# Optimization experiments

Measured on AMD Instinct MI355X. Metric: run time of the kernel, lower is better.

The kernel has to match this reference:

```python
import jax, jax.numpy as jnp
import numpy as np

B, L, HIDDEN = 64, 200, 256
HEADS = 8
MAX_WIDTH = 5
EPS = 1e-5  # F.layer_norm default eps


def _ln(x):
    # F.layer_norm with no learned affine
    m = jnp.mean(x, axis=-1, keepdims=True)
    v = jnp.mean((x - m) ** 2, axis=-1, keepdims=True)
    return (x - m) * jax.lax.rsqrt(v + EPS)


def _area_pool(x, max_width, mode):
    # x: [B, H, L, D] -> pooled spans of widths 1..max_width (valid windows),
    # concatenated along the memory axis: M = sum_w (L - w + 1)
    Lx = x.shape[2]
    outs = []
    for w in range(1, max_width + 1):
        # [w, B, H, L-w+1, D] stack of shifted slices (w <= 5, tiny loop)
        win = jnp.stack([x[:, :, i:Lx - w + 1 + i, :] for i in range(w)], axis=0)
        if mode == 'max':
            outs.append(win.max(axis=0))
        elif mode == 'mean':
            outs.append(win.mean(axis=0))
        else:  # 'sum'
            outs.append(win.sum(axis=0))
    return jnp.concatenate(outs, axis=2)


def _mha_area(q_in, k_in, v_in, Wq, bq, Wk, bk, Wv, bv, Wo, bo):
    # per-head size equals hidden_size (key_query_size_hidden = hidden_size)
    Bq, Lq, _ = q_in.shape
    Dh = Wq.shape[1] // HEADS

    def split(x):
        return x.reshape(x.shape[0], x.shape[1], HEADS, Dh).transpose(0, 2, 1, 3)

    q = split(q_in @ Wq + bq)  # [B, H, Lq, Dh]
    k = split(k_in @ Wk + bk)
    v = split(v_in @ Wv + bv)
    k_area = _area_pool(k, MAX_WIDTH, 'max')   # aggr='max' key pooling
    v_area = _area_pool(v, MAX_WIDTH, 'sum')   # values pooled by sum (t2t default)
    scale = jnp.asarray(1.0 / np.sqrt(Dh), q.dtype)
    logits = jnp.einsum('bhqd,bhmd->bhqm', q, k_area) * scale
    attn = jax.nn.softmax(logits, axis=-1)  # dropout inactive at eval
    out = jnp.einsum('bhqm,bhmd->bhqd', attn, v_area)
    out = out.transpose(0, 2, 1, 3).reshape(Bq, Lq, HEADS * Dh)
    return out @ Wo + bo


def setup_inputs() -> dict:
    key = jax.random.key(0)
    ks = jax.random.split(key, 16)
    stdv = 1.0 / np.sqrt(HIDDEN)
    u = lambda k, shp: jax.random.uniform(k, shp, jnp.float32, -stdv, stdv)
    HD = HEADS * HIDDEN  # 2048
    return {
        'A': jax.random.normal(ks[0], (B, L, L), jnp.float32),
        'hidden': jax.random.normal(ks[1], (B, L, HIDDEN), jnp.float32),
        'Wq': u(ks[2], (HIDDEN, HD)), 'bq': u(ks[3], (HD,)),
        'Wk': u(ks[4], (HIDDEN, HD)), 'bk': u(ks[5], (HD,)),
        'Wv': u(ks[6], (HIDDEN, HD)), 'bv': u(ks[7], (HD,)),
        'Wo': u(ks[8], (HD, HIDDEN)), 'bo': u(ks[9], (HIDDEN,)),
        'W1': u(ks[10], (HIDDEN, 4 * HIDDEN)), 'b1': u(ks[11], (4 * HIDDEN,)),
        'W2': u(ks[12], (4 * HIDDEN, HIDDEN)), 'b2': u(ks[13], (HIDDEN,)),
    }


def reference(A, hidden, Wq, bq, Wk, bk, Wv, bv, Wo, bo, W1, b1, W2, b2):
    # step = 1 -> single ATTNCell; A is unused by ATTNCell (matches source)
    attn1 = _mha_area(hidden, hidden, hidden, Wq, bq, Wk, bk, Wv, bv, Wo, bo)
    attn1 = _ln(attn1 + hidden)
    attn2 = _mha_area(attn1, hidden, hidden, Wq, bq, Wk, bk, Wv, bv, Wo, bo)
    attn2 = _ln(attn1 + attn2)  # F.dropout inactive (eval)
    x = jax.nn.relu(attn2 @ W1 + b1) @ W2 + b2
    return _ln(attn2 + x)
```

## Files before the change

kernel.cpp:

```cpp
#include <hip/hip_runtime.h>
#include <hip/hip_bf16.h>
#include <cstdint>
#include <cstddef>

#define BATCH 64
#define LSEQ 200
#define HID 256
#define NH 8
#define DH 256
#define HD (NH*DH)
#define MROWS (BATCH*LSEQ)
#define EPS 1e-5f
#define CSCALE 0.09014195f

typedef unsigned short ushort_t;
typedef __attribute__((ext_vector_type(8))) short bf16x8;
typedef __attribute__((ext_vector_type(8))) unsigned short u16x8;
typedef __attribute__((ext_vector_type(4))) float f32x4;

__device__ __forceinline__ float b2f(ushort_t u) {
    union { unsigned int i; float f; } c; c.i = ((unsigned int)u) << 16; return c.f;
}
__device__ __forceinline__ ushort_t f2b(float f) {
    __hip_bfloat16 h = __float2bfloat16(f);
    union { __hip_bfloat16 h; ushort_t u; } c; c.h = h; return c.u;
}
__device__ __forceinline__ ushort_t f2b_trunc(float f) {
    return (ushort_t)(__float_as_uint(f) >> 16);
}
__device__ __forceinline__ float to_f32(float x) { return x; }
__device__ __forceinline__ float to_f32(ushort_t x) { return b2f(x); }
__device__ __forceinline__ void store_val(float* p, float v) { *p = v; }
__device__ __forceinline__ void store_val(ushort_t* p, float v) { *p = f2b(v); }

__device__ __forceinline__ u16x8 bmax8(u16x8 a, u16x8 b) {
    union U { u16x8 v; __hip_bfloat162 h[4]; };
    U ua, ub, r; ua.v = a; ub.v = b;
    #pragma unroll
    for (int i = 0; i < 4; ++i) r.h[i] = __hmax2(ua.h[i], ub.h[i]);
    return r.v;
}
__device__ __forceinline__ u16x8 badd8(u16x8 a, u16x8 b) {
    union U { u16x8 v; __hip_bfloat162 h[4]; };
    U ua, ub, r; ua.v = a; ub.v = b;
    #pragma unroll
    for (int i = 0; i < 4; ++i) r.h[i] = __hadd2(ua.h[i], ub.h[i]);
    return r.v;
}

__device__ __forceinline__ void gll16(const void* g, void* l) {
    __builtin_amdgcn_global_load_lds(
        (const __attribute__((address_space(1))) unsigned int*)g,
        (__attribute__((address_space(3))) unsigned int*)l, 16, 0, 0);
}

template<bool RELU, int OMODE, bool SCALEC>
__global__ __launch_bounds__(256) void gemm_bt(
    const ushort_t* __restrict__ A, const ushort_t* __restrict__ Bt,
    const float* __restrict__ bias, ushort_t* __restrict__ C,
    int M, int N, int K)
{
    __shared__ ushort_t As[128 * 32];
    __shared__ ushort_t Bs[128 * 32];
    const int t = threadIdx.x;
    const int m0 = blockIdx.y * 128, n0 = blockIdx.x * 128;
    const int wave = t >> 6, lane = t & 63;
    const int l15 = lane & 15, lq = lane >> 4;
    const int wr = wave >> 1, wc = wave & 1;

    f32x4 acc[4][4];
    #pragma unroll
    for (int i = 0; i < 4; ++i)
        #pragma unroll
        for (int j = 0; j < 4; ++j) acc[i][j] = (f32x4){0.f, 0.f, 0.f, 0.f};

    for (int k0 = 0; k0 < K; k0 += 32) {
        __syncthreads();
        #pragma unroll
        for (int i = 0; i < 2; ++i) {
            int li = i * 256 + t;
            int ml = li >> 2, cp = li & 3;
            int cg = cp ^ ((ml ^ (ml >> 2)) & 3);
            gll16(A + (size_t)(m0 + ml) * K + k0 + cg * 8, &As[li * 8]);
        }
        #pragma unroll
        for (int i = 0; i < 2; ++i) {
            int li = i * 256 + t;
            int nl = li >> 2, cp = li & 3;
            int cg = cp ^ ((nl ^ (nl >> 2)) & 3);
            gll16(Bt + (size_t)(n0 + nl) * K + k0 + cg * 8, &Bs[li * 8]);
        }
        __syncthreads();
        bf16x8 af[4], bfr[4];
        #pragma unroll
        for (int i = 0; i < 4; ++i) {
            int r = wr * 64 + i * 16 + l15;
            int pc = lq ^ ((r ^ (r >> 2)) & 3);
            af[i] = *(const bf16x8*)&As[r * 32 + pc * 8];
        }
        #pragma unroll
        for (int j = 0; j < 4; ++j) {
            int r = wc * 64 + j * 16 + l15;
            int pc = lq ^ ((r ^ (r >> 2)) & 3);
            bfr[j] = *(const bf16x8*)&Bs[r * 32 + pc * 8];
        }
        #pragma unroll
        for (int i = 0; i < 4; ++i)
            #pragma unroll
            for (int j = 0; j < 4; ++j)
                acc[i][j] = __builtin_amdgcn_mfma_f32_16x16x32_bf16(af[i], bfr[j], acc[i][j], 0, 0, 0);
    }
    if (OMODE == 2) {
        #pragma unroll
        for (int i = 0; i < 4; ++i) {
            int mbase = m0 + wr * 64 + i * 16 + 4 * lq;
            int bb = (int)(((unsigned)mbase * 5243u) >> 20);
            int ll = mbase - bb * 200;
            #pragma unroll
            for (int j = 0; j < 4; ++j) {
                int n = n0 + wc * 64 + j * 16 + l15;
                float bsv = bias[n];
                ushort4 o4;
                o4.x = f2b(acc[i][j][0] + bsv); o4.y = f2b(acc[i][j][1] + bsv);
                o4.z = f2b(acc[i][j][2] + bsv); o4.w = f2b(acc[i][j][3] + bsv);
                size_t addr = ((size_t)(bb * NH + (n >> 8)) * 256 + (n & 255)) * LSEQ + ll;
                *(ushort4*)&C[addr] = o4;
            }
        }
    } else {
        #pragma unroll
        for (int i = 0; i < 4; ++i) {
            #pragma unroll
            for (int e = 0; e < 4; ++e) {
                int m = m0 + wr * 64 + i * 16 + 4 * lq + e;
                #pragma unroll
                for (int j = 0; j < 4; ++j) {
                    int n = n0 + wc * 64 + j * 16 + l15;
                    float v = acc[i][j][e] + bias[n];
                    if (RELU) v = fmaxf(v, 0.f);
                    if (SCALEC) v *= CSCALE;
                    if (OMODE == 1) {
                        int bb = (int)(((unsigned)m * 5243u) >> 20);
                        int ll = m - bb * 200;
                        size_t addr = ((((size_t)(bb * NH + (n >> 8))) * LSEQ + ll) << 8) + (n & 255);
                        C[addr] = f2b(v);
                    } else {
                        C[(size_t)m * N + n] = f2b(v);
                    }
                }
            }
        }
    }
}

__global__ __launch_bounds__(512, 2) void attn_mfma11(
    const ushort_t* __restrict__ Q, const ushort_t* __restrict__ Khm,
    const ushort_t* __restrict__ Vt, ushort_t* __restrict__ O)
{
    const int id = blockIdx.x;
    const int xcd = id & 7, slot_ = id >> 3;
    const int qt = slot_ & 1;
    const int bh = ((slot_ >> 1) << 3) + xcd;
    const int b = bh >> 3, h = bh & 7;
    const int q0 = qt * 128;
    const int t = threadIdx.x;
    const int wave = t >> 6, lane = t & 63;
    const int l15 = lane & 15, lq = lane >> 4;

    __shared__ ushort_t Ks[64 * 256];
    __shared__ ushort_t Vs[256 * 64];
    __shared__ ushort_t Ps[8][16][72];

    const ushort_t* kbh = Khm + (size_t)bh * LSEQ * DH;
    const ushort_t* vtb = Vt + (size_t)bh * DH * LSEQ;
    const ushort_t* qbh = Q + ((size_t)b * LSEQ) * HD + h * DH;
    const int qrow = q0 + wave * 16 + l15;

    bf16x8 qf[8];
    if (qrow < LSEQ) {
        const ushort_t* qp = qbh + (size_t)qrow * HD + 8 * lq;
        #pragma unroll
        for (int g = 0; g < 8; ++g) qf[g] = *(const bf16x8*)(qp + 32 * g);
    } else {
        bf16x8 zf = {0,0,0,0,0,0,0,0};
        #pragma unroll
        for (int g = 0; g < 8; ++g) qf[g] = zf;
    }

    f32x4 oacc[16];
    #pragma unroll
    for (int i = 0; i < 16; ++i) oacc[i] = (f32x4){0.f, 0.f, 0.f, 0.f};
    float l_st[4];
    #pragma unroll
    for (int e = 0; e < 4; ++e) l_st[e] = 0.f;

    const int dc = t & 31, mb = t >> 5;
    const int vd = t >> 1, vh = t & 1;

    auto step = [&](bool tail) {
        f32x4 sacc[4];
        #pragma unroll
        for (int ms = 0; ms < 4; ++ms) {
            f32x4 s = (f32x4){0.f, 0.f, 0.f, 0.f};
            const int row = ms * 16 + l15;
            #pragma unroll
            for (int g = 0; g < 8; ++g) {
                const int phys = (lq + 4 * g) ^ l15;
                s = __builtin_amdgcn_mfma_f32_16x16x32_bf16(
                        qf[g], *(const bf16x8*)&Ks[row * 256 + phys * 8], s, 0, 0, 0);
            }
            sacc[ms] = s;
        }
        if (tail) {
            #pragma unroll
            for (int ms = 0; ms < 4; ++ms) {
                const int slot = ms * 16 + l15;
                const bool inval = ((slot & 7) > 7 - (slot >> 3)) || ((slot >> 3) > 4);
                #pragma unroll
                for (int e = 0; e < 4; ++e)
                    if (inval) sacc[ms][e] = -1e30f;
            }
        }
        #pragma unroll
        for (int ms = 0; ms < 4; ++ms)
            #pragma unroll
            for (int e = 0; e < 4; ++e) {
                float pj = __builtin_exp2f(sacc[ms][e]);
                l_st[e] += pj;
                Ps[wave][4 * lq + e][ms * 16 + l15] = f2b_trunc(pj);
            }

        bf16x8 pf0 = *(const bf16x8*)&Ps[wave][l15][8 * lq];
        bf16x8 pf1 = *(const bf16x8*)&Ps[wave][l15][32 + 8 * lq];
        #pragma unroll
        for (int dt = 0; dt < 16; ++dt) {
            const int d = dt * 16 + l15;
            const int p0 = lq ^ (d & 7);
            const int p1 = (lq + 4) ^ (d & 7);
            oacc[dt] = __builtin_amdgcn_mfma_f32_16x16x32_bf16(
                           pf0, *(const bf16x8*)&Vs[d * 64 + p0 * 8], oacc[dt], 0, 0, 0);
            oacc[dt] = __builtin_amdgcn_mfma_f32_16x16x32_bf16(
                           pf1, *(const bf16x8*)&Vs[d * 64 + p1 * 8], oacc[dt], 0, 0, 0);
        }
    };

    for (int ti = 0; ti < 3; ++ti) {
        const int st0 = ti * 64;
        #pragma unroll
        for (int cls = 0; cls < 5; ++cls) {
            u16x8 kf[4];
            #pragma unroll
            for (int k4 = 0; k4 < 4; ++k4)
                kf[k4] = *(const u16x8*)(kbh + (size_t)(st0 + mb + 16 * k4 + cls) * DH + dc * 8);
            __syncthreads();

            #pragma unroll
            for (int k4 = 0; k4 < 4; ++k4) {
                int m = mb + 16 * k4;
                ushort_t* kp = &Ks[m * 256 + ((dc ^ (m & 15)) * 8)];
                *(u16x8*)kp = (cls == 0) ? kf[k4] : bmax8(*(const u16x8*)kp, kf[k4]);
            }
            {
                const ushort_t* vrow = vtb + (size_t)vd * LSEQ + st0 + vh * 32;
                u16x8 vc[5];
                #pragma unroll
                for (int c = 0; c < 5; ++c) vc[c] = *(const u16x8*)(vrow + c * 8);
                #pragma unroll
                for (int cl = 0; cl < 4; ++cl) {
                    const int cg = vh * 4 + cl;
                    ushort_t* vp = &Vs[vd * 64 + ((cg ^ (vd & 7)) * 8)];
                    if (cls == 0) {
                        *(u16x8*)vp = vc[cl];
                    } else {
                        u16x8 sh;
                        #pragma unroll
                        for (int j = 0; j < 8; ++j)
                            sh[j] = (j + cls < 8) ? vc[cl][j + cls] : vc[cl + 1][j + cls - 8];
                        *(u16x8*)vp = badd8(*(const u16x8*)vp, sh);
                    }
                }
            }
            __syncthreads();
            step(false);
        }
    }

    {
        __syncthreads();
        if (mb < 8) {
            u16x8 krun = *(const u16x8*)(kbh + (size_t)(192 + mb) * DH + dc * 8);
            const u16x8 kz = {0,0,0,0,0,0,0,0};
            #pragma unroll
            for (int k8 = 0; k8 < 8; ++k8) {
                const bool v = (k8 <= 4) && (mb <= 7 - k8);
                if (k8 > 0 && v)
                    krun = bmax8(krun, *(const u16x8*)(kbh + (size_t)(192 + mb + k8) * DH + dc * 8));
                int slot = k8 * 8 + mb;
                *(u16x8*)&Ks[slot * 256 + ((dc ^ (slot & 15)) * 8)] = v ? krun : kz;
            }
        }
        {
            u16x8 v0 = *(const u16x8*)(vtb + (size_t)vd * LSEQ + 192);
            float f[8], s[8];
            #pragma unroll
            for (int e = 0; e < 8; ++e) { f[e] = b2f(v0[e]); s[e] = f[e]; }
            #pragma unroll
            for (int cl = 0; cl < 4; ++cl) {
                const int c = vh * 4 + cl;
                u16x8 ov = {0,0,0,0,0,0,0,0};
                if (c <= 4) {
                    #pragma unroll
                    for (int u = 1; u <= 4; ++u)
                        if (u <= c)
                            #pragma unroll
                            for (int off = 0; off < 8; ++off)
                                if (off <= 7 - u && u == c)
                                    ;
                    #pragma unroll
                    for (int j = 0; j < 8; ++j) {
                        if (j <= 7 - c) {
                            float acc = 0.f;
                            #pragma unroll
                            for (int u = 0; u <= 4; ++u)
                                if (u <= c) acc += f[j + u];
                            ov[j] = f2b(acc);
                        }
                    }
                }
                *(u16x8*)&Vs[vd * 64 + ((c ^ (vd & 7)) * 8)] = ov;
            }
        }
        __syncthreads();
        step(true);
    }

    #pragma unroll
    for (int off = 1; off < 16; off <<= 1)
        #pragma unroll
        for (int e = 0; e < 4; ++e) l_st[e] += __shfl_xor(l_st[e], off);

    ushort_t* ob = O + ((size_t)b * LSEQ) * HD + h * DH;
    #pragma unroll
    for (int e = 0; e < 4; ++e) {
        const int q = q0 + wave * 16 + 4 * lq + e;
        if (q < LSEQ) {
            const float linv = 1.f / l_st[e];
            #pragma unroll
            for (int dt = 0; dt < 16; ++dt)
                ob[(size_t)q * HD + dt * 16 + l15] = f2b(oacc[dt][e] * linv);
        }
    }
}

template<typename TR, typename TO>
__global__ __launch_bounds__(256) void residual_ln(
    const ushort_t* __restrict__ X, const TR* __restrict__ R, TO* __restrict__ Out)
{
    const int row = blockIdx.x;
    const int t = threadIdx.x;
    const size_t base = (size_t)row * HID;
    float v = b2f(X[base + t]) + to_f32(R[base + t]);
    float s = v, q = v * v;
    #pragma unroll
    for (int o = 32; o > 0; o >>= 1) {
        s += __shfl_xor(s, o, 64);
        q += __shfl_xor(q, o, 64);
    }
    __shared__ float ss[4], sq[4];
    const int wave = t >> 6, lane = t & 63;
    if (lane == 0) { ss[wave] = s; sq[wave] = q; }
    __syncthreads();
    s = ss[0] + ss[1] + ss[2] + ss[3];
    q = sq[0] + sq[1] + sq[2] + sq[3];
    float mean = s * (1.f / HID);
    float var  = q * (1.f / HID) - mean * mean;
    store_val(&Out[base + t], (v - mean) * rsqrtf(var + EPS));
}

__global__ __launch_bounds__(256) void cvt_f32_bf16(const float* __restrict__ in,
                                                    ushort_t* __restrict__ out) {
    const int i = (blockIdx.x * 256 + threadIdx.x) * 4;
    float4 v = *(const float4*)(in + i);
    ushort4 o;
    o.x = f2b(v.x); o.y = f2b(v.y); o.z = f2b(v.z); o.w = f2b(v.w);
    *(ushort4*)(out + i) = o;
}

__global__ __launch_bounds__(256) void wtrans(const float* __restrict__ W,
                                              ushort_t* __restrict__ Wt, int K, int N) {
    __shared__ float tile[32][33];
    const int t = threadIdx.x;
    const int tx = t & 31, ty = t >> 5;
    const int n0 = blockIdx.x * 32, k0 = blockIdx.y * 32;
    #pragma unroll
    for (int s = 0; s < 4; ++s)
        tile[ty + 8 * s][tx] = W[(size_t)(k0 + ty + 8 * s) * N + n0 + tx];
    __syncthreads();
    #pragma unroll
    for (int s = 0; s < 4; ++s)
        Wt[(size_t)(n0 + ty + 8 * s) * K + k0 + tx] = f2b(tile[tx][ty + 8 * s]);
}

extern "C" void kernel_launch(void* const* d_in, const int* in_sizes, int n_in,
                              void* d_out, int out_size, void* d_ws, size_t ws_size,
                              hipStream_t stream) {
    const float* hidden = (const float*)d_in[1];
    const float* Wq = (const float*)d_in[2];  const float* bq = (const float*)d_in[3];
    const float* Wk = (const float*)d_in[4];  const float* bk = (const float*)d_in[5];
    const float* Wv = (const float*)d_in[6];  const float* bv = (const float*)d_in[7];
    const float* Wo = (const float*)d_in[8];  const float* bo = (const float*)d_in[9];
    const float* W1 = (const float*)d_in[10]; const float* b1 = (const float*)d_in[11];
    const float* W2 = (const float*)d_in[12]; const float* b2 = (const float*)d_in[13];
    float* out = (float*)d_out;

    constexpr size_t SZ_BF   = (size_t)MROWS * HD * 2;
    constexpr size_t SZ_HBF  = (size_t)MROWS * HID * 2;
    constexpr size_t SZ_WQKV = (size_t)HID * HD * 2;
    constexpr size_t SZ_W12  = (size_t)HID * 4 * HID * 2;
    char* ws = (char*)d_ws;
    size_t off = 0;
    ushort_t* kb   = (ushort_t*)(ws + off); off += SZ_BF;
    ushort_t* vt   = (ushort_t*)(ws + off); off += SZ_BF;
    ushort_t* qo   = (ushort_t*)(ws + off); off += SZ_BF;
    ushort_t* hb   = (ushort_t*)(ws + off); off += SZ_HBF;
    ushort_t* at1  = (ushort_t*)(ws + off); off += SZ_HBF;
    ushort_t* at2  = (ushort_t*)(ws + off); off += SZ_HBF;
    ushort_t* proj = (ushort_t*)(ws + off); off += SZ_HBF;
    ushort_t* WtQ  = (ushort_t*)(ws + off); off += SZ_WQKV;
    ushort_t* WtK  = (ushort_t*)(ws + off); off += SZ_WQKV;
    ushort_t* WtV  = (ushort_t*)(ws + off); off += SZ_WQKV;
    ushort_t* WtO  = (ushort_t*)(ws + off); off += SZ_WQKV;
    ushort_t* Wt1  = (ushort_t*)(ws + off); off += SZ_W12;
    ushort_t* Wt2  = (ushort_t*)(ws + off); off += SZ_W12;
    if (ws_size < off) return;
    ushort_t* ffn1 = qo;

    dim3 blk(256);
    cvt_f32_bf16<<<MROWS * HID / 1024, blk, 0, stream>>>(hidden, hb);
    wtrans<<<dim3(HD / 32, HID / 32), blk, 0, stream>>>(Wq, WtQ, HID, HD);
    wtrans<<<dim3(HD / 32, HID / 32), blk, 0, stream>>>(Wk, WtK, HID, HD);
    wtrans<<<dim3(HD / 32, HID / 32), blk, 0, stream>>>(Wv, WtV, HID, HD);
    wtrans<<<dim3(HID / 32, HD / 32), blk, 0, stream>>>(Wo, WtO, HD, HID);
    wtrans<<<dim3(4 * HID / 32, HID / 32), blk, 0, stream>>>(W1, Wt1, HID, 4 * HID);
    wtrans<<<dim3(HID / 32, 4 * HID / 32), blk, 0, stream>>>(W2, Wt2, 4 * HID, HID);

    const dim3 gProj(HD / 128, MROWS / 128);
    const dim3 gOut(HID / 128, MROWS / 128);
    const dim3 gF1(4 * HID / 128, MROWS / 128);

    gemm_bt<false, 1, false><<<gProj, blk, 0, stream>>>(hb, WtK, bk, kb, MROWS, HD, HID);
    gemm_bt<false, 2, false><<<gProj, blk, 0, stream>>>(hb, WtV, bv, vt, MROWS, HD, HID);

    gemm_bt<false, 0, true><<<gProj, blk, 0, stream>>>(hb, WtQ, bq, qo, MROWS, HD, HID);
    attn_mfma11<<<2 * BATCH * NH, 512, 0, stream>>>(qo, kb, vt, qo);
    gemm_bt<false, 0, false><<<gOut, blk, 0, stream>>>(qo, WtO, bo, proj, MROWS, HID, HD);
    residual_ln<float, ushort_t><<<MROWS, blk, 0, stream>>>(proj, hidden, at1);

    gemm_bt<false, 0, true><<<gProj, blk, 0, stream>>>(at1, WtQ, bq, qo, MROWS, HD, HID);
    attn_mfma11<<<2 * BATCH * NH, 512, 0, stream>>>(qo, kb, vt, qo);
    gemm_bt<false, 0, false><<<gOut, blk, 0, stream>>>(qo, WtO, bo, proj, MROWS, HID, HD);
    residual_ln<ushort_t, ushort_t><<<MROWS, blk, 0, stream>>>(proj, at1, at2);

    gemm_bt<true, 0, false><<<gF1, blk, 0, stream>>>(at2, Wt1, b1, ffn1, MROWS, 4 * HID, HID);
    gemm_bt<false, 0, false><<<gOut, blk, 0, stream>>>(ffn1, Wt2, b2, proj, MROWS, HID, 4 * HID);
    residual_ln<ushort_t, float><<<MROWS, blk, 0, stream>>>(proj, at2, out);
}
```

Before: 984.5 us.

## Double-buffer pooled K/V tiles in LDS and prefetch next global loads

The attention kernel now keeps two LDS buffers each for the max-pooled K tile and the sum-pooled V tile. Each width class builds its pooled tile in one buffer from the previous buffer, which drops the leading __syncthreads per step. Global loads of the next class's K rows, and of the next tile's V rows, are issued after the LDS writes so their latency overlaps the synchronisation and MFMA work. The tail tile preloads its K rows into registers instead of loading inside the running-max loop. The cost is roughly 64 KB more LDS per block, which can limit how many blocks fit on a CU, and more live registers for the prefetched fragments.

```diff
diff --git a/kernel.cpp b/kernel.cpp
--- a/kernel.cpp
+++ b/kernel.cpp
@@ -153,7 +153,7 @@
     }
 }
 
-__global__ __launch_bounds__(512, 2) void attn_mfma11(
+__global__ __launch_bounds__(512, 2) void attn_mfma12(
     const ushort_t* __restrict__ Q, const ushort_t* __restrict__ Khm,
     const ushort_t* __restrict__ Vt, ushort_t* __restrict__ O)
 {
@@ -167,8 +167,8 @@
     const int wave = t >> 6, lane = t & 63;
     const int l15 = lane & 15, lq = lane >> 4;
 
-    __shared__ ushort_t Ks[64 * 256];
-    __shared__ ushort_t Vs[256 * 64];
+    __shared__ ushort_t Ks[2][64 * 256];
+    __shared__ ushort_t Vs[2][256 * 64];
     __shared__ ushort_t Ps[8][16][72];
 
     const ushort_t* kbh = Khm + (size_t)bh * LSEQ * DH;
@@ -197,7 +197,7 @@
     const int dc = t & 31, mb = t >> 5;
     const int vd = t >> 1, vh = t & 1;
 
-    auto step = [&](bool tail) {
+    auto step = [&](const ushort_t* KB, const ushort_t* VB, bool tail) {
         f32x4 sacc[4];
         #pragma unroll
         for (int ms = 0; ms < 4; ++ms) {
@@ -207,7 +207,7 @@
             for (int g = 0; g < 8; ++g) {
                 const int phys = (lq + 4 * g) ^ l15;
                 s = __builtin_amdgcn_mfma_f32_16x16x32_bf16(
-                        qf[g], *(const bf16x8*)&Ks[row * 256 + phys * 8], s, 0, 0, 0);
+                        qf[g], *(const bf16x8*)&KB[row * 256 + phys * 8], s, 0, 0, 0);
             }
             sacc[ms] = s;
         }
@@ -238,100 +238,112 @@
             const int p0 = lq ^ (d & 7);
             const int p1 = (lq + 4) ^ (d & 7);
             oacc[dt] = __builtin_amdgcn_mfma_f32_16x16x32_bf16(
-                           pf0, *(const bf16x8*)&Vs[d * 64 + p0 * 8], oacc[dt], 0, 0, 0);
+                           pf0, *(const bf16x8*)&VB[d * 64 + p0 * 8], oacc[dt], 0, 0, 0);
             oacc[dt] = __builtin_amdgcn_mfma_f32_16x16x32_bf16(
-                           pf1, *(const bf16x8*)&Vs[d * 64 + p1 * 8], oacc[dt], 0, 0, 0);
+                           pf1, *(const bf16x8*)&VB[d * 64 + p1 * 8], oacc[dt], 0, 0, 0);
         }
     };
+
+    u16x8 kf[4], vc[5];
+    {
+        const ushort_t* vrow = vtb + (size_t)vd * LSEQ + vh * 32;
+        #pragma unroll
+        for (int c = 0; c < 5; ++c) vc[c] = *(const u16x8*)(vrow + c * 8);
+        #pragma unroll
+        for (int k4 = 0; k4 < 4; ++k4)
+            kf[k4] = *(const u16x8*)(kbh + (size_t)(mb + 16 * k4) * DH + dc * 8);
+    }
 
     for (int ti = 0; ti < 3; ++ti) {
         const int st0 = ti * 64;
         #pragma unroll
         for (int cls = 0; cls < 5; ++cls) {
-            u16x8 kf[4];
-            #pragma unroll
-            for (int k4 = 0; k4 < 4; ++k4)
-                kf[k4] = *(const u16x8*)(kbh + (size_t)(st0 + mb + 16 * k4 + cls) * DH + dc * 8);
-            __syncthreads();
+            const int buf = (ti + cls) & 1;
+            ushort_t* kc = &Ks[buf][0];  const ushort_t* kp = &Ks[buf ^ 1][0];
+            ushort_t* vcu = &Vs[buf][0]; const ushort_t* vp = &Vs[buf ^ 1][0];
 
             #pragma unroll
             for (int k4 = 0; k4 < 4; ++k4) {
                 int m = mb + 16 * k4;
-                ushort_t* kp = &Ks[m * 256 + ((dc ^ (m & 15)) * 8)];
-                *(u16x8*)kp = (cls == 0) ? kf[k4] : bmax8(*(const u16x8*)kp, kf[k4]);
-            }
-            {
-                const ushort_t* vrow = vtb + (size_t)vd * LSEQ + st0 + vh * 32;
-                u16x8 vc[5];
+                int off = m * 256 + ((dc ^ (m & 15)) * 8);
+                *(u16x8*)(kc + off) = (cls == 0) ? kf[k4]
+                                                 : bmax8(*(const u16x8*)(kp + off), kf[k4]);
+            }
+            #pragma unroll
+            for (int cl = 0; cl < 4; ++cl) {
+                int cg = vh * 4 + cl;
+                int off = vd * 64 + ((cg ^ (vd & 7)) * 8);
+                if (cls == 0) {
+                    *(u16x8*)(vcu + off) = vc[cl];
+                } else {
+                    u16x8 sh;
+                    #pragma unroll
+                    for (int j = 0; j < 8; ++j)
+                        sh[j] = (j + cls < 8) ? vc[cl][j + cls] : vc[cl + 1][j + cls - 8];
+                    *(u16x8*)(vcu + off) = badd8(*(const u16x8*)(vp + off), sh);
+                }
+            }
+            if (cls < 4) {
+                #pragma unroll
+                for (int k4 = 0; k4 < 4; ++k4)
+                    kf[k4] = *(const u16x8*)(kbh + (size_t)(st0 + mb + 16 * k4 + cls + 1) * DH + dc * 8);
+            } else if (ti < 2) {
+                const ushort_t* vrow = vtb + (size_t)vd * LSEQ + (st0 + 64) + vh * 32;
                 #pragma unroll
                 for (int c = 0; c < 5; ++c) vc[c] = *(const u16x8*)(vrow + c * 8);
                 #pragma unroll
-                for (int cl = 0; cl < 4; ++cl) {
-                    const int cg = vh * 4 + cl;
-                    ushort_t* vp = &Vs[vd * 64 + ((cg ^ (vd & 7)) * 8)];
-                    if (cls == 0) {
-                        *(u16x8*)vp = vc[cl];
-                    } else {
-                        u16x8 sh;
-                        #pragma unroll
-                        for (int j = 0; j < 8; ++j)
-                            sh[j] = (j + cls < 8) ? vc[cl][j + cls] : vc[cl + 1][j + cls - 8];
-                        *(u16x8*)vp = badd8(*(const u16x8*)vp, sh);
-                    }
-                }
+                for (int k4 = 0; k4 < 4; ++k4)
+                    kf[k4] = *(const u16x8*)(kbh + (size_t)(st0 + 64 + mb + 16 * k4) * DH + dc * 8);
             }
             __syncthreads();
-            step(false);
+            step(kc, vcu, false);
         }
     }
 
     {
-        __syncthreads();
+        ushort_t* kc = &Ks[1][0];
+        ushort_t* vcu = &Vs[1][0];
         if (mb < 8) {
-            u16x8 krun = *(const u16x8*)(kbh + (size_t)(192 + mb) * DH + dc * 8);
+            u16x8 kt[5];
+            #pragma unroll
+            for (int k = 0; k < 5; ++k)
+                kt[k] = *(const u16x8*)(kbh + (size_t)(192 + mb + k) * DH + dc * 8);
+            u16x8 krun = kt[0];
             const u16x8 kz = {0,0,0,0,0,0,0,0};
             #pragma unroll
             for (int k8 = 0; k8 < 8; ++k8) {
                 const bool v = (k8 <= 4) && (mb <= 7 - k8);
-                if (k8 > 0 && v)
-                    krun = bmax8(krun, *(const u16x8*)(kbh + (size_t)(192 + mb + k8) * DH + dc * 8));
+                if (k8 > 0 && k8 <= 4 && v) krun = bmax8(krun, kt[k8]);
                 int slot = k8 * 8 + mb;
-                *(u16x8*)&Ks[slot * 256 + ((dc ^ (slot & 15)) * 8)] = v ? krun : kz;
+                *(u16x8*)(kc + slot * 256 + ((dc ^ (slot & 15)) * 8)) = v ? krun : kz;
             }
         }
         {
             u16x8 v0 = *(const u16x8*)(vtb + (size_t)vd * LSEQ + 192);
-            float f[8], s[8];
-            #pragma unroll
-            for (int e = 0; e < 8; ++e) { f[e] = b2f(v0[e]); s[e] = f[e]; }
+            float f[8];
+            #pragma unroll
+            for (int e = 0; e < 8; ++e) f[e] = b2f(v0[e]);
             #pragma unroll
             for (int cl = 0; cl < 4; ++cl) {
                 const int c = vh * 4 + cl;
                 u16x8 ov = {0,0,0,0,0,0,0,0};
                 if (c <= 4) {
                     #pragma unroll
-                    for (int u = 1; u <= 4; ++u)
-                        if (u <= c)
-                            #pragma unroll
-                            for (int off = 0; off < 8; ++off)
-                                if (off <= 7 - u && u == c)
-                                    ;
-                    #pragma unroll
                     for (int j = 0; j < 8; ++j) {
                         if (j <= 7 - c) {
-                            float acc = 0.f;
+                            float a = 0.f;
                             #pragma unroll
                             for (int u = 0; u <= 4; ++u)
-                                if (u <= c) acc += f[j + u];
-                            ov[j] = f2b(acc);
+                                if (u <= c) a += f[j + u];
+                            ov[j] = f2b(a);
                         }
                     }
                 }
-                *(u16x8*)&Vs[vd * 64 + ((c ^ (vd & 7)) * 8)] = ov;
+                *(u16x8*)(vcu + vd * 64 + ((c ^ (vd & 7)) * 8)) = ov;
             }
         }
         __syncthreads();
-        step(true);
+        step(kc, vcu, true);
     }
 
     #pragma unroll
@@ -452,12 +464,12 @@
     gemm_bt<false, 2, false><<<gProj, blk, 0, stream>>>(hb, WtV, bv, vt, MROWS, HD, HID);
 
     gemm_bt<false, 0, true><<<gProj, blk, 0, stream>>>(hb, WtQ, bq, qo, MROWS, HD, HID);
-    attn_mfma11<<<2 * BATCH * NH, 512, 0, stream>>>(qo, kb, vt, qo);
+    attn_mfma12<<<2 * BATCH * NH, 512, 0, stream>>>(qo, kb, vt, qo);
     gemm_bt<false, 0, false><<<gOut, blk, 0, stream>>>(qo, WtO, bo, proj, MROWS, HID, HD);
     residual_ln<float, ushort_t><<<MROWS, blk, 0, stream>>>(proj, hidden, at1);
 
     gemm_bt<false, 0, true><<<gProj, blk, 0, stream>>>(at1, WtQ, bq, qo, MROWS, HD, HID);
-    attn_mfma11<<<2 * BATCH * NH, 512, 0, stream>>>(qo, kb, vt, qo);
+    attn_mfma12<<<2 * BATCH * NH, 512, 0, stream>>>(qo, kb, vt, qo);
     gemm_bt<false, 0, false><<<gOut, blk, 0, stream>>>(qo, WtO, bo, proj, MROWS, HID, HD);
     residual_ln<ushort_t, ushort_t><<<MROWS, blk, 0, stream>>>(proj, at1, at2);
 
```

Result: slower. 1.578 ms (+60.3%).
